# Kernel tuning notes

Hardware: AMD Instinct MI355X
Metric: run time of the kernel (lower is better)

Reference implementation:

```python
import jax, jax.numpy as jnp
import numpy as np

VOCAB = 10000
X_DIM = 128
HID = 256


def setup_inputs() -> dict:
    key = jax.random.key(0)
    ks = jax.random.split(key, 8)
    B, S = 128, 50
    x = jax.random.randint(ks[0], (B, S), 0, VOCAB, dtype=jnp.int32).astype(jnp.int64)
    emb = jax.random.normal(ks[1], (VOCAB, X_DIM), dtype=jnp.float32) * 0.02
    # PyTorch nn.RNN params: W_ih [H, X], W_hh [H, H], b_ih [H], b_hh [H]
    W_ih = jax.random.normal(ks[2], (HID, X_DIM), dtype=jnp.float32) * (1.0 / np.sqrt(HID))
    W_hh = jax.random.normal(ks[3], (HID, HID), dtype=jnp.float32) * (1.0 / np.sqrt(HID))
    b_ih = jax.random.normal(ks[4], (HID,), dtype=jnp.float32) * 0.01
    b_hh = jax.random.normal(ks[5], (HID,), dtype=jnp.float32) * 0.01
    # nn.Linear: W_aff [V, H], b_aff [V]
    W_aff = jax.random.normal(ks[6], (VOCAB, HID), dtype=jnp.float32) * (1.0 / np.sqrt(HID))
    b_aff = jax.random.normal(ks[7], (VOCAB,), dtype=jnp.float32) * 0.01
    return {"x": x, "emb": emb, "W_ih": W_ih, "W_hh": W_hh,
            "b_ih": b_ih, "b_hh": b_hh, "W_aff": W_aff, "b_aff": b_aff}


def reference(x, emb, W_ih, W_hh, b_ih, b_hh, W_aff, b_aff):
    B, S = x.shape
    embs = emb[x]                                    # [B, S, X]
    # Precompute input projection for all timesteps (batched GEMM)
    xin = jnp.einsum('bsx,hx->bsh', embs, W_ih) + b_ih + b_hh  # [B, S, H]
    h0 = jnp.zeros((B, HID), dtype=embs.dtype)

    def step(h, xt):
        h = jnp.tanh(xt + h @ W_hh.T)
        return h, h

    _, hs = jax.lax.scan(step, h0, jnp.swapaxes(xin, 0, 1))  # hs: [S, B, H]
    hs = jnp.swapaxes(hs, 0, 1)                              # [B, S, H]
    ys = jnp.einsum('bsh,vh->bsv', hs, W_aff) + b_aff        # [B, S, V]
    return ys
```

## Files before the change

kernel.cpp:

```cpp
#include <hip/hip_runtime.h>
#include <hip/hip_bf16.h>
#include <stdint.h>

#define VOCAB 10000
#define XDIM 128
#define HID 256
#define BATCH 128
#define SEQ 50
#define ROWS (BATCH * SEQ)

#define BM 128
#define BN 256
#define BK 64
#define NTM 50
#define NTN 40

typedef __bf16 bf16x8 __attribute__((ext_vector_type(8)));
typedef float f32x4 __attribute__((ext_vector_type(4)));

__device__ __forceinline__ uint16_t f2bf(float f) {
    union { float f; uint32_t i; } v;
    v.f = f;
    uint32_t x = v.i;
    return (uint16_t)((x + 0x7fffu + ((x >> 16) & 1u)) >> 16);
}

__global__ __launch_bounds__(256) void k0_cast(
    const float* __restrict__ src, uint16_t* __restrict__ dst) {
    const int i = (blockIdx.x * 256 + threadIdx.x) * 8;
    float4 a = *(const float4*)(src + i);
    float4 b = *(const float4*)(src + i + 4);
    uint16_t t[8];
    t[0] = f2bf(a.x); t[1] = f2bf(a.y); t[2] = f2bf(a.z); t[3] = f2bf(a.w);
    t[4] = f2bf(b.x); t[5] = f2bf(b.y); t[6] = f2bf(b.z); t[7] = f2bf(b.w);
    *(uint4*)(dst + i) = *(const uint4*)t;
}

__global__ __launch_bounds__(256, 2) void k1_xin(
    const int* __restrict__ x, const float* __restrict__ emb,
    const float* __restrict__ Wih, const float* __restrict__ bih,
    const float* __restrict__ bhh, float* __restrict__ xin) {
    __shared__ __align__(16) float es[8][XDIM];
    const int r0 = blockIdx.x * 8;
    const int tid = threadIdx.x;

    {
        const int row = tid >> 5, c = tid & 31;
        const int tok = x[r0 + row];
        *(float4*)&es[row][c * 4] = *(const float4*)(emb + tok * XDIM + c * 4);
    }
    __syncthreads();

    const int j = tid;
    float wf[XDIM];
    const float4* wrow = (const float4*)(Wih + j * XDIM);
#pragma unroll
    for (int c = 0; c < 32; ++c) *(float4*)&wf[c * 4] = wrow[c];
    const float bias = bih[j] + bhh[j];

    float acc[8];
#pragma unroll
    for (int r = 0; r < 8; ++r) acc[r] = bias;
#pragma unroll
    for (int k4 = 0; k4 < 32; ++k4) {
#pragma unroll
        for (int r = 0; r < 8; ++r) {
            float4 e = *(const float4*)&es[r][k4 * 4];
            acc[r] += e.x * wf[k4 * 4 + 0] + e.y * wf[k4 * 4 + 1] +
                      e.z * wf[k4 * 4 + 2] + e.w * wf[k4 * 4 + 3];
        }
    }
#pragma unroll
    for (int r = 0; r < 8; ++r) xin[(r0 + r) * HID + j] = acc[r];
}

__global__ __launch_bounds__(512, 2) void k2_rnn(
    const float* __restrict__ xin, const float* __restrict__ Whh,
    uint16_t* __restrict__ hs) {
    __shared__ __align__(16) float hb[HID];
    __shared__ float ps[HID];
    const int b = blockIdx.x;
    const int j = threadIdx.x & 255;
    const int half = threadIdx.x >> 8;

    float wh[128];
    const float4* wrow = (const float4*)(Whh + j * HID + half * 128);
#pragma unroll
    for (int c = 0; c < 32; ++c) *(float4*)&wh[c * 4] = wrow[c];

    if (threadIdx.x < HID) hb[threadIdx.x] = 0.0f;
    __syncthreads();

    const float* xr = xin + b * SEQ * HID;
    uint16_t* hr = hs + b * SEQ * HID;

    for (int t = 0; t < SEQ; ++t) {
        const float xv = xr[t * HID + j];
        const float4* h4 = (const float4*)(hb + half * 128);
        float a0 = 0.f, a1 = 0.f, a2 = 0.f, a3 = 0.f;
#pragma unroll
        for (int c = 0; c < 32; ++c) {
            float4 v = h4[c];
            a0 += v.x * wh[c * 4 + 0];
            a1 += v.y * wh[c * 4 + 1];
            a2 += v.z * wh[c * 4 + 2];
            a3 += v.w * wh[c * 4 + 3];
        }
        const float part = (a0 + a1) + (a2 + a3);
        if (half) ps[j] = part;
        __syncthreads();
        if (!half) {
            const float hn = tanhf(part + ps[j] + xv);
            hb[j] = hn;
            hr[t * HID + j] = f2bf(hn);
        }
        __syncthreads();
    }
}

__global__ __launch_bounds__(256, 2) void k3_gemm(
    const uint16_t* __restrict__ A,
    const uint16_t* __restrict__ Bw,
    const float* __restrict__ baff,
    float* __restrict__ out) {
    __shared__ __align__(16) char smem[49152];
    uint16_t* As = (uint16_t*)smem;
    uint16_t* Bs = (uint16_t*)(smem + BM * BK * 2);

    const int bid0 = blockIdx.x;
    const int bid = (bid0 & 7) * ((NTM * NTN) / 8) + (bid0 >> 3);
    const int bm = bid % NTM, bn = bid / NTM;
    const int m0 = bm * BM, n0 = bn * BN;
    const int tid = threadIdx.x;
    const int wv = tid >> 6, ln = tid & 63;
    const int wm = wv & 1, wn = wv >> 1;
    const int quad = ln >> 4, l15 = ln & 15;

    f32x4 acc[4][8];
#pragma unroll
    for (int i = 0; i < 4; ++i)
#pragma unroll
        for (int jj = 0; jj < 8; ++jj) acc[i][jj] = (f32x4)0.0f;

    const int lrow = ln >> 3;
    const int gsw = ((ln & 7) ^ lrow) * 8;

    for (int kt = 0; kt < 4; ++kt) {
        const int k0 = kt * BK;
#pragma unroll
        for (int i = 0; i < 4; ++i) {
            const int ci = wv * 4 + i;
            const uint16_t* g = A + (size_t)(m0 + ci * 8 + lrow) * HID + k0 + gsw;
            __builtin_amdgcn_global_load_lds(
                (const __attribute__((address_space(1))) void*)g,
                (__attribute__((address_space(3))) void*)(As + ci * 512), 16, 0, 0);
        }
#pragma unroll
        for (int i = 0; i < 8; ++i) {
            const int ci = wv * 8 + i;
            int n = n0 + ci * 8 + lrow;
            if (n > VOCAB - 1) n = VOCAB - 1;
            const uint16_t* g = Bw + (size_t)n * HID + k0 + gsw;
            __builtin_amdgcn_global_load_lds(
                (const __attribute__((address_space(1))) void*)g,
                (__attribute__((address_space(3))) void*)(Bs + ci * 512), 16, 0, 0);
        }
        __syncthreads();

#pragma unroll
        for (int kk = 0; kk < 2; ++kk) {
            const int gk = kk * 4 + quad;
            bf16x8 af[4], bf[8];
#pragma unroll
            for (int tm = 0; tm < 4; ++tm) {
                const int R = wm * 64 + tm * 16 + l15;
                af[tm] = *(const bf16x8*)&As[R * 64 + ((gk ^ (R & 7)) * 8)];
            }
#pragma unroll
            for (int tn = 0; tn < 8; ++tn) {
                const int R = wn * 128 + tn * 16 + l15;
                bf[tn] = *(const bf16x8*)&Bs[R * 64 + ((gk ^ (R & 7)) * 8)];
            }
#pragma unroll
            for (int tm = 0; tm < 4; ++tm)
#pragma unroll
                for (int tn = 0; tn < 8; ++tn)
                    acc[tm][tn] = __builtin_amdgcn_mfma_f32_16x16x32_bf16(
                        af[tm], bf[tn], acc[tm][tn], 0, 0, 0);
        }
        __syncthreads();
    }

    float* csw = (float*)smem + wv * 16 * 132;
    float bias[8];
#pragma unroll
    for (int tn = 0; tn < 8; ++tn) {
        int n = n0 + wn * 128 + tn * 16 + l15;
        bias[tn] = baff[n > VOCAB - 1 ? VOCAB - 1 : n];
    }
#pragma unroll
    for (int tm = 0; tm < 4; ++tm) {
#pragma unroll
        for (int tn = 0; tn < 8; ++tn)
#pragma unroll
            for (int r = 0; r < 4; ++r)
                csw[(quad * 4 + r) * 132 + tn * 16 + l15] =
                    acc[tm][tn][r] + bias[tn];
        __syncthreads();
#pragma unroll
        for (int it = 0; it < 8; ++it) {
            const int row = it * 2 + (ln >> 5);
            const int c4 = (ln & 31) * 4;
            const f32x4 v = *(const f32x4*)&csw[row * 132 + c4];
            const int gm = m0 + wm * 64 + tm * 16 + row;
            const int gn = n0 + wn * 128 + c4;
            if (gn < VOCAB)
                __builtin_nontemporal_store(
                    v, (f32x4*)(out + (size_t)gm * VOCAB + gn));
        }
        __syncthreads();
    }
}

extern "C" void kernel_launch(void* const* d_in, const int* in_sizes, int n_in,
                              void* d_out, int out_size, void* d_ws, size_t ws_size,
                              hipStream_t stream) {
    const int* x = (const int*)d_in[0];
    const float* emb = (const float*)d_in[1];
    const float* Wih = (const float*)d_in[2];
    const float* Whh = (const float*)d_in[3];
    const float* bih = (const float*)d_in[4];
    const float* bhh = (const float*)d_in[5];
    const float* Waff = (const float*)d_in[6];
    const float* baff = (const float*)d_in[7];

    float* xin = (float*)d_ws;
    uint16_t* hsb = (uint16_t*)((char*)d_ws + (size_t)ROWS * HID * 4);
    uint16_t* Wb = hsb + (size_t)ROWS * HID;
    float* out = (float*)d_out;

    k0_cast<<<(VOCAB * HID) / (256 * 8), 256, 0, stream>>>(Waff, Wb);
    k1_xin<<<ROWS / 8, 256, 0, stream>>>(x, emb, Wih, bih, bhh, xin);
    k2_rnn<<<BATCH, 512, 0, stream>>>(xin, Whh, hsb);
    k3_gemm<<<NTM * NTN, 256, 0, stream>>>(hsb, Wb, baff, out);
}
```

Before: 363.4 us.

## Double-buffer LDS tiles in output GEMM with BK=32 prefetch

The vocabulary GEMM now splits K into eight 32-wide steps and keeps two LDS buffers, issuing the global-to-LDS loads for the next K step before running the MFMAs on the current one. This is meant to hide global load latency behind compute instead of stalling on a barrier after every load. LDS footprint stays within the existing 48KB, and the swizzle pattern is reworked for 32-element rows. Risk: the loop has one barrier per step, and no explicit wait on the async loads is visible before the data is consumed, so correctness relies on the barrier's implicit wait. The smaller K step also means less MFMA work per barrier.

New measurement: 371.7 us. 1.02x slower.

```diff
diff --git a/kernel.cpp b/kernel.cpp
--- a/kernel.cpp
+++ b/kernel.cpp
@@ -11,7 +11,8 @@
 
 #define BM 128
 #define BN 256
-#define BK 64
+#define BK 32
+#define NKT (HID / BK)
 #define NTM 50
 #define NTN 40
 
@@ -125,7 +126,7 @@
     float* __restrict__ out) {
     __shared__ __align__(16) char smem[49152];
     uint16_t* As = (uint16_t*)smem;
-    uint16_t* Bs = (uint16_t*)(smem + BM * BK * 2);
+    uint16_t* Bs = (uint16_t*)(smem + 2 * BM * BK * 2);
 
     const int bid0 = blockIdx.x;
     const int bid = (bid0 & 7) * ((NTM * NTN) / 8) + (bid0 >> 3);
@@ -142,54 +143,74 @@
 #pragma unroll
         for (int jj = 0; jj < 8; ++jj) acc[i][jj] = (f32x4)0.0f;
 
-    const int lrow = ln >> 3;
-    const int gsw = ((ln & 7) ^ lrow) * 8;
-
-    for (int kt = 0; kt < 4; ++kt) {
-        const int k0 = kt * BK;
-#pragma unroll
-        for (int i = 0; i < 4; ++i) {
-            const int ci = wv * 4 + i;
-            const uint16_t* g = A + (size_t)(m0 + ci * 8 + lrow) * HID + k0 + gsw;
-            __builtin_amdgcn_global_load_lds(
-                (const __attribute__((address_space(1))) void*)g,
-                (__attribute__((address_space(3))) void*)(As + ci * 512), 16, 0, 0);
-        }
-#pragma unroll
-        for (int i = 0; i < 8; ++i) {
-            const int ci = wv * 8 + i;
-            int n = n0 + ci * 8 + lrow;
-            if (n > VOCAB - 1) n = VOCAB - 1;
-            const uint16_t* g = Bw + (size_t)n * HID + k0 + gsw;
-            __builtin_amdgcn_global_load_lds(
-                (const __attribute__((address_space(1))) void*)g,
-                (__attribute__((address_space(3))) void*)(Bs + ci * 512), 16, 0, 0);
-        }
-        __syncthreads();
-
-#pragma unroll
-        for (int kk = 0; kk < 2; ++kk) {
-            const int gk = kk * 4 + quad;
-            bf16x8 af[4], bf[8];
-#pragma unroll
-            for (int tm = 0; tm < 4; ++tm) {
-                const int R = wm * 64 + tm * 16 + l15;
-                af[tm] = *(const bf16x8*)&As[R * 64 + ((gk ^ (R & 7)) * 8)];
-            }
-#pragma unroll
-            for (int tn = 0; tn < 8; ++tn) {
-                const int R = wn * 128 + tn * 16 + l15;
-                bf[tn] = *(const bf16x8*)&Bs[R * 64 + ((gk ^ (R & 7)) * 8)];
-            }
-#pragma unroll
-            for (int tm = 0; tm < 4; ++tm)
-#pragma unroll
-                for (int tn = 0; tn < 8; ++tn)
-                    acc[tm][tn] = __builtin_amdgcn_mfma_f32_16x16x32_bf16(
-                        af[tm], bf[tn], acc[tm][tn], 0, 0, 0);
-        }
-        __syncthreads();
-    }
+    const int lrow = ln >> 2;
+    const int gsw = ((ln & 3) ^ ((ln >> 3) & 3)) * 8;
+
+    int bnrow[4];
+#pragma unroll
+    for (int i = 0; i < 4; ++i) {
+        int n = n0 + (wv * 4 + i) * 16 + lrow;
+        bnrow[i] = n > VOCAB - 1 ? VOCAB - 1 : n;
+    }
+
+#define STAGE(kt, buf)                                                        \
+    do {                                                                      \
+        const int k0_ = (kt) * BK;                                            \
+        uint16_t* Asb_ = As + (buf) * (BM * BK);                              \
+        uint16_t* Bsb_ = Bs + (buf) * (BN * BK);                              \
+        _Pragma("unroll")                                                     \
+        for (int i_ = 0; i_ < 2; ++i_) {                                      \
+            const int ci_ = wv * 2 + i_;                                      \
+            const uint16_t* g_ =                                              \
+                A + (size_t)(m0 + ci_ * 16 + lrow) * HID + k0_ + gsw;         \
+            __builtin_amdgcn_global_load_lds(                                 \
+                (const __attribute__((address_space(1))) void*)g_,            \
+                (__attribute__((address_space(3))) void*)(Asb_ + ci_ * 512),  \
+                16, 0, 0);                                                    \
+        }                                                                     \
+        _Pragma("unroll")                                                     \
+        for (int i_ = 0; i_ < 4; ++i_) {                                      \
+            const int ci_ = wv * 4 + i_;                                      \
+            const uint16_t* g_ =                                              \
+                Bw + (size_t)bnrow[i_] * HID + k0_ + gsw;                     \
+            __builtin_amdgcn_global_load_lds(                                 \
+                (const __attribute__((address_space(1))) void*)g_,            \
+                (__attribute__((address_space(3))) void*)(Bsb_ + ci_ * 512),  \
+                16, 0, 0);                                                    \
+        }                                                                     \
+    } while (0)
+
+    STAGE(0, 0);
+    __syncthreads();
+
+#pragma unroll
+    for (int kt = 0; kt < NKT; ++kt) {
+        const int cur = kt & 1;
+        if (kt < NKT - 1) STAGE(kt + 1, cur ^ 1);
+
+        const uint16_t* Asb = As + cur * (BM * BK);
+        const uint16_t* Bsb = Bs + cur * (BN * BK);
+        bf16x8 af[4], bf[8];
+#pragma unroll
+        for (int tm = 0; tm < 4; ++tm) {
+            const int R = wm * 64 + tm * 16 + l15;
+            af[tm] = *(const bf16x8*)&Asb[R * 32 + ((quad ^ ((R >> 1) & 3)) * 8)];
+        }
+#pragma unroll
+        for (int tn = 0; tn < 8; ++tn) {
+            const int R = wn * 128 + tn * 16 + l15;
+            bf[tn] = *(const bf16x8*)&Bsb[R * 32 + ((quad ^ ((R >> 1) & 3)) * 8)];
+        }
+#pragma unroll
+        for (int tm = 0; tm < 4; ++tm)
+#pragma unroll
+            for (int tn = 0; tn < 8; ++tn)
+                acc[tm][tn] = __builtin_amdgcn_mfma_f32_16x16x32_bf16(
+                    af[tm], bf[tn], acc[tm][tn], 0, 0, 0);
+
+        __syncthreads();
+    }
+#undef STAGE
 
     float* csw = (float*)smem + wv * 16 * 132;
     float bias[8];
```
